# Kernel optimization log

Measured on AMD Instinct MI355X. Metric: run time of the kernel, lower is better.

## Reference

```python
import jax, jax.numpy as jnp
import numpy as np

B, S, D = 2, 1024, 4096
H, KV, HD = 32, 8, 128
GROUP = H // KV


def qlinear(x, w_int8, w_scale, bias):
    """Int8 dynamic-activation-quant linear: per-row activation scale, per-out-channel weight scale."""
    K = x.shape[-1]
    xf = x.reshape(-1, K)
    sx = jnp.max(jnp.abs(xf), axis=1, keepdims=True) / 127.0  # [M,1]
    sx = jnp.where(sx == 0, jnp.float32(1.0), sx)
    xi = jax.lax.stop_gradient(jnp.clip(jnp.round(xf / sx), -127.0, 127.0)).astype(jnp.int8)
    y = jnp.matmul(xi.astype(jnp.int32), w_int8.T.astype(jnp.int32)).astype(jnp.float32)  # int32 accum
    y = y * sx * w_scale[None, :]
    if bias is not None:
        y = y + bias
    return y.reshape(x.shape[:-1] + (w_int8.shape[0],))


def rope(t, c, s):
    half = t.shape[-1] // 2
    rot = jnp.concatenate([-t[..., half:], t[..., :half]], axis=-1)
    return t * c + rot * s


def setup_inputs() -> dict:
    key = jax.random.key(0)
    ks = jax.random.split(key, 10)
    x = jax.random.normal(ks[0], (B, S, D), dtype=jnp.float32)
    # RoPE tables (full-head_dim rotate-half convention)
    inv = 1.0 / (10000.0 ** (jnp.arange(0, HD, 2, dtype=jnp.float32) / HD))
    ang = jnp.arange(S, dtype=jnp.float32)[:, None] * inv[None, :]  # [S, HD/2]
    cos = jnp.concatenate([jnp.cos(ang), jnp.cos(ang)], axis=-1)
    sin = jnp.concatenate([jnp.sin(ang), jnp.sin(ang)], axis=-1)
    d_kv = KV * HD
    wq = jax.random.randint(ks[1], (H * HD, D), -127, 128, dtype=jnp.int32).astype(jnp.int8)
    wk = jax.random.randint(ks[2], (d_kv, D), -127, 128, dtype=jnp.int32).astype(jnp.int8)
    wv = jax.random.randint(ks[3], (d_kv, D), -127, 128, dtype=jnp.int32).astype(jnp.int8)
    wo = jax.random.randint(ks[4], (D, H * HD), -127, 128, dtype=jnp.int32).astype(jnp.int8)
    sc_in = jnp.float32(1.0 / (127.0 * np.sqrt(D)))
    sc_o = jnp.float32(1.0 / (127.0 * np.sqrt(H * HD)))
    sq = jnp.full((H * HD,), sc_in, dtype=jnp.float32)
    sk = jnp.full((d_kv,), sc_in, dtype=jnp.float32)
    sv = jnp.full((d_kv,), sc_in, dtype=jnp.float32)
    so = jnp.full((D,), sc_o, dtype=jnp.float32)
    bq = 0.01 * jax.random.normal(ks[5], (H * HD,), dtype=jnp.float32)
    bk = 0.01 * jax.random.normal(ks[6], (d_kv,), dtype=jnp.float32)
    bv = 0.01 * jax.random.normal(ks[7], (d_kv,), dtype=jnp.float32)
    return {"x": x, "cos": cos, "sin": sin, "wq": wq, "sq": sq, "bq": bq,
            "wk": wk, "sk": sk, "bk": bk, "wv": wv, "sv": sv, "bv": bv,
            "wo": wo, "so": so}


def reference(x, cos, sin, wq, sq, bq, wk, sk, bk, wv, sv, bv, wo, so):
    b, seq, _ = x.shape
    q = qlinear(x, wq, sq, bq).reshape(b, seq, H, HD)
    k = qlinear(x, wk, sk, bk).reshape(b, seq, KV, HD)
    v = qlinear(x, wv, sv, bv).reshape(b, seq, KV, HD)
    c = cos[:seq][None, :, None, :]
    s = sin[:seq][None, :, None, :]
    q = rope(q, c, s)
    k = rope(k, c, s)
    # start_pos=0 prefill: cache write then slice-back is identity -> use k, v directly.
    # GQA broadcast: q_head_to_kv_head = h // group_size
    idx = jnp.arange(H) // GROUP
    kf = k[:, :, idx, :]  # [b, seq, H, HD]
    vf = v[:, :, idx, :]
    scores = jnp.einsum('bqhd,bkhd->bhqk', q, kf) / jnp.sqrt(jnp.float32(HD))
    causal = jnp.tril(jnp.ones((seq, seq), dtype=bool))
    scores = jnp.where(causal[None, None, :, :], scores, jnp.float32(-jnp.inf))
    probs = jax.nn.softmax(scores, axis=-1)
    out = jnp.einsum('bhqk,bkhd->bqhd', probs, vf).reshape(b, seq, H * HD)
    return qlinear(out, wo, so, None)
```

## Files before the change

kernel.cpp:

```cpp
#include <hip/hip_runtime.h>


#define B_   2
#define S_   1024
#define D_   4096
#define H_   32
#define KV_  8
#define HD_  128
#define NR   (B_ * S_)
#define NQKV (H_*HD_ + 2*KV_*HD_)

#define KSTR 132
#define VSTR 68

typedef __attribute__((ext_vector_type(8))) short  short8;
typedef __attribute__((ext_vector_type(4))) float  f32x4;
typedef __attribute__((ext_vector_type(4))) int    int4v;

static __device__ __forceinline__ unsigned short f2bf(float f) {
    unsigned u = __builtin_bit_cast(unsigned, f);
    u += 0x7fffu + ((u >> 16) & 1u);
    return (unsigned short)(u >> 16);
}

static __device__ __forceinline__ void async_cp16(const void* g, void* l) {
    __builtin_amdgcn_global_load_lds(
        (const __attribute__((address_space(1))) void*)g,
        (__attribute__((address_space(3))) void*)l, 16, 0, 0);
}

__global__ __launch_bounds__(256) void quantize_rows_k(
    const float* __restrict__ X, signed char* __restrict__ Xq,
    float* __restrict__ sx_out)
{
    int row = blockIdx.x;
    const f32x4* xr = (const f32x4*)(X + (size_t)row * 4096);
    int t = threadIdx.x;

    f32x4 v[4];
    #pragma unroll
    for (int i = 0; i < 4; i++) v[i] = xr[t + i * 256];

    float m = 0.f;
    #pragma unroll
    for (int i = 0; i < 4; i++)
        #pragma unroll
        for (int j = 0; j < 4; j++) m = fmaxf(m, fabsf(v[i][j]));
    #pragma unroll
    for (int off = 32; off > 0; off >>= 1) m = fmaxf(m, __shfl_down(m, off, 64));
    __shared__ float red[4];
    if ((t & 63) == 0) red[t >> 6] = m;
    __syncthreads();
    float mm = fmaxf(fmaxf(red[0], red[1]), fmaxf(red[2], red[3]));
    float sx = mm / 127.0f;
    if (sx == 0.f) sx = 1.f;
    if (t == 0) sx_out[row] = sx;

    int* dst = (int*)(Xq + (size_t)row * 4096);
    #pragma unroll
    for (int i = 0; i < 4; i++) {
        int o = 0;
        #pragma unroll
        for (int j = 0; j < 4; j++) {
            float q = rintf(v[i][j] / sx);
            q = fminf(fmaxf(q, -127.f), 127.f);
            o |= (((int)q) & 0xff) << (j * 8);
        }
        dst[t + i * 256] = o;
    }
}

__global__ __launch_bounds__(256) void convert_all_w(
    const int* __restrict__ wq, const int* __restrict__ wk,
    const int* __restrict__ wv, const int* __restrict__ wo,
    signed char* __restrict__ Wqkv, signed char* __restrict__ Wo)
{
    int i = blockIdx.x * 256 + threadIdx.x;
    const int* src;
    signed char* dst;
    if (i < 1048576)      { src = wq + (size_t)i * 16;              dst = Wqkv + (size_t)i * 16; }
    else if (i < 1310720) { int j = i - 1048576; src = wk + (size_t)j * 16; dst = Wqkv + 16777216 + (size_t)j * 16; }
    else if (i < 1572864) { int j = i - 1310720; src = wv + (size_t)j * 16; dst = Wqkv + 20971520 + (size_t)j * 16; }
    else                  { int j = i - 1572864; src = wo + (size_t)j * 16; dst = Wo + (size_t)j * 16; }
    const int4v* s4 = (const int4v*)src;
    int4v a = s4[0], b = s4[1], c = s4[2], d = s4[3];
    int4v o;
    o[0] = (a[0]&0xff) | ((a[1]&0xff)<<8) | ((a[2]&0xff)<<16) | ((a[3]&0xff)<<24);
    o[1] = (b[0]&0xff) | ((b[1]&0xff)<<8) | ((b[2]&0xff)<<16) | ((b[3]&0xff)<<24);
    o[2] = (c[0]&0xff) | ((c[1]&0xff)<<8) | ((c[2]&0xff)<<16) | ((c[3]&0xff)<<24);
    o[3] = (d[0]&0xff) | ((d[1]&0xff)<<8) | ((d[2]&0xff)<<16) | ((d[3]&0xff)<<24);
    *(int4v*)dst = o;
}

template<int MODE>
__global__ __launch_bounds__(256) void gemm_i8_k(
    const signed char* __restrict__ A, const signed char* __restrict__ Bm,
    float* __restrict__ C, const float* __restrict__ rs,
    const float* __restrict__ cs, int K, int lda, int ldb, int ldc)
{
    __shared__ __align__(16) signed char As[128 * 128];
    __shared__ __align__(16) signed char Bs[128 * 128];

    int t    = threadIdx.x;
    int m0   = blockIdx.y * 128;
    int n0   = blockIdx.x * 128;
    int lane = t & 63;
    int w    = t >> 6;
    int wm   = (w >> 1) * 64;
    int wn   = (w & 1) * 64;
    int l15  = lane & 15;
    int quad = lane >> 4;

    int4v acc[4][4];
    #pragma unroll
    for (int i = 0; i < 4; i++)
        #pragma unroll
        for (int j = 0; j < 4; j++) { int4v z = {0,0,0,0}; acc[i][j] = z; }

    int cw   = w * 64 + lane;
    int smr  = cw >> 3;
    int scol = cw & 7;

    for (int k0 = 0; k0 < K; k0 += 128) {
        #pragma unroll
        for (int p = 0; p < 4; ++p) {
            int m  = p * 32 + smr;
            int kc = scol ^ (m & 7);
            const signed char* ga = A  + (size_t)(m0 + m) * lda + k0 + kc * 16;
            const signed char* gb = Bm + (size_t)(n0 + m) * ldb + k0 + kc * 16;
            async_cp16(ga, As + (p * 256 + w * 64) * 16);
            async_cp16(gb, Bs + (p * 256 + w * 64) * 16);
        }
        __syncthreads();

        #pragma unroll
        for (int ks = 0; ks < 2; ks++) {
            int4v af[4], bf[4];
            #pragma unroll
            for (int i = 0; i < 4; i++) {
                int ra = wm + i*16 + l15;
                int rb = wn + i*16 + l15;
                af[i] = *(const int4v*)&As[(ra * 8 + (((ks*4 + quad) ^ (ra & 7)))) * 16];
                bf[i] = *(const int4v*)&Bs[(rb * 8 + (((ks*4 + quad) ^ (rb & 7)))) * 16];
            }
            #pragma unroll
            for (int i = 0; i < 4; i++)
                #pragma unroll
                for (int j = 0; j < 4; j++)
                    acc[i][j] = __builtin_amdgcn_mfma_i32_16x16x64_i8(af[i], bf[j], acc[i][j], 0, 0, 0);
        }
        __syncthreads();
    }

    #pragma unroll
    for (int i = 0; i < 4; i++) {
        #pragma unroll
        for (int j = 0; j < 4; j++) {
            #pragma unroll
            for (int r = 0; r < 4; r++) {
                int row = m0 + wm + i*16 + quad*4 + r;
                int col = n0 + wn + j*16 + l15;
                float v = (float)acc[i][j][r];
                if (MODE == 3) v *= rs[row] * cs[col];
                C[(size_t)row * ldc + col] = v;
            }
        }
    }
}

__global__ __launch_bounds__(256) void derope_k(
    const float* __restrict__ Y, const float* __restrict__ sx,
    const float* __restrict__ sq, const float* __restrict__ bq,
    const float* __restrict__ sk, const float* __restrict__ bk,
    const float* __restrict__ sv, const float* __restrict__ bv,
    const float* __restrict__ cosb, const float* __restrict__ sinb,
    unsigned short* __restrict__ Q, unsigned short* __restrict__ Kb,
    unsigned short* __restrict__ Vt)
{
    const float qs = 0.08838834764831845f;
    int r = blockIdx.x;
    int b = r >> 10;
    int s = r & (S_ - 1);
    float sxr = sx[r];
    const float* yr = Y + (size_t)r * NQKV;
    int t = threadIdx.x;

    for (int p = t; p < H_ * 64; p += 256) {
        int h = p >> 6, d = p & 63;
        int ca = h * HD_ + d;
        float a  = yr[ca]      * sxr * sq[ca]      + bq[ca];
        float b2 = yr[ca + 64] * sxr * sq[ca + 64] + bq[ca + 64];
        float c  = cosb[s * HD_ + d], sn = sinb[s * HD_ + d];
        size_t base = (((size_t)(b * H_ + h)) * S_ + s) * HD_;
        Q[base + d]      = f2bf((a * c - b2 * sn) * qs);
        Q[base + d + 64] = f2bf((b2 * c + a * sn) * qs);
    }
    for (int p = t; p < KV_ * 64; p += 256) {
        int kv = p >> 6, d = p & 63;
        int ci = kv * HD_ + d;
        int ca = H_ * HD_ + ci;
        float a  = yr[ca]      * sxr * sk[ci]      + bk[ci];
        float b2 = yr[ca + 64] * sxr * sk[ci + 64] + bk[ci + 64];
        float c  = cosb[s * HD_ + d], sn = sinb[s * HD_ + d];
        size_t base = (((size_t)(b * KV_ + kv)) * S_ + s) * HD_;
        Kb[base + d]      = f2bf(a * c - b2 * sn);
        Kb[base + d + 64] = f2bf(b2 * c + a * sn);
    }
    for (int p = t; p < KV_ * HD_; p += 256) {
        int kv = p >> 7, d = p & 127;
        int ci = kv * HD_ + d;
        int ca = H_ * HD_ + KV_ * HD_ + ci;
        float v = yr[ca] * sxr * sv[ci] + bv[ci];
        size_t idx = (((size_t)(b * KV_ + kv)) * HD_ + d) * S_ + s;
        Vt[idx] = f2bf(v);
    }
}

__global__ __launch_bounds__(256) void flash_attn_k(
    const unsigned short* __restrict__ Qg,
    const unsigned short* __restrict__ Kg,
    const unsigned short* __restrict__ Vg,
    float* __restrict__ O)
{
    __shared__ __align__(16) unsigned short Ks[64 * KSTR];
    __shared__ __align__(16) unsigned short Vs[HD_ * VSTR];

    int pair = blockIdx.x;
    int qt   = 15 - blockIdx.y;
    int b    = pair >> 5;
    int kv   = (pair & 31) >> 2;

    const unsigned short* Qb = Qg + ((size_t)pair * S_ + qt * 64) * HD_;
    const unsigned short* Kbp = Kg + ((size_t)(b * KV_ + kv)) * (S_ * HD_);
    const unsigned short* Vb = Vg + ((size_t)(b * KV_ + kv)) * (HD_ * S_);

    int t    = threadIdx.x;
    int lane = t & 63;
    int w    = t >> 6;
    int l15  = lane & 15;
    int quad = lane >> 4;

    short8 qf[4];
    #pragma unroll
    for (int ks = 0; ks < 4; ks++)
        qf[ks] = *(const short8*)(Qb + (size_t)(w*16 + l15) * HD_ + ks*32 + quad*8);

    f32x4 oacc[8];
    #pragma unroll
    for (int n = 0; n < 8; n++) { f32x4 z = {0.f,0.f,0.f,0.f}; oacc[n] = z; }
    float mrow[4], lrow[4];
    #pragma unroll
    for (int r = 0; r < 4; r++) { mrow[r] = -1e30f; lrow[r] = 0.f; }

    int kr4 = t >> 4, kc = t & 15;
    int vr4 = t >> 3, vc = t & 7;

    for (int j = 0; j <= qt; ++j) {
        int k0 = j * 64;
        __syncthreads();

        #pragma unroll
        for (int p = 0; p < 4; ++p) {
            int krow = p * 16 + kr4;
            short8 kd = *(const short8*)(Kbp + (size_t)(k0 + krow) * HD_ + kc * 8);
            *(short8*)&Ks[krow * KSTR + kc * 8] = kd;
            int vrow = p * 32 + vr4;
            short8 vd = *(const short8*)(Vb + (size_t)vrow * S_ + k0 + vc * 8);
            *(short8*)&Vs[vrow * VSTR + vc * 8] = vd;
        }
        __syncthreads();

        f32x4 sacc[4];
        #pragma unroll
        for (int n = 0; n < 4; n++) { f32x4 z = {0.f,0.f,0.f,0.f}; sacc[n] = z; }
        #pragma unroll
        for (int n = 0; n < 4; n++) {
            #pragma unroll
            for (int ks = 0; ks < 4; ks++) {
                short8 kf = *(const short8*)&Ks[(n*16 + l15) * KSTR + ks*32 + quad*8];
                sacc[n] = __builtin_amdgcn_mfma_f32_16x16x32_bf16(qf[ks], kf, sacc[n], 0, 0, 0);
            }
        }

        if (j == qt) {
            #pragma unroll
            for (int n = 0; n < 4; n++)
                #pragma unroll
                for (int r = 0; r < 4; r++) {
                    int qrow = w*16 + quad*4 + r;
                    int kcol = n*16 + l15;
                    if (kcol > qrow) sacc[n][r] = -1e30f;
                }
        }

        #pragma unroll
        for (int r = 0; r < 4; r++) {
            float mx = fmaxf(fmaxf(sacc[0][r], sacc[1][r]), fmaxf(sacc[2][r], sacc[3][r]));
            mx = fmaxf(mx, __shfl_xor(mx, 1, 64));
            mx = fmaxf(mx, __shfl_xor(mx, 2, 64));
            mx = fmaxf(mx, __shfl_xor(mx, 4, 64));
            mx = fmaxf(mx, __shfl_xor(mx, 8, 64));
            float mnew = fmaxf(mrow[r], mx);
            float alpha = __expf(mrow[r] - mnew);
            mrow[r] = mnew;
            float s = 0.f;
            #pragma unroll
            for (int n = 0; n < 4; n++) {
                float e = __expf(sacc[n][r] - mnew);
                sacc[n][r] = e;
                s += e;
            }
            s += __shfl_xor(s, 1, 64);
            s += __shfl_xor(s, 2, 64);
            s += __shfl_xor(s, 4, 64);
            s += __shfl_xor(s, 8, 64);
            lrow[r] = lrow[r] * alpha + s;
            #pragma unroll
            for (int n = 0; n < 8; n++) oacc[n][r] *= alpha;
        }

        __syncthreads();

        unsigned short* Ps = Ks;
        #pragma unroll
        for (int n = 0; n < 4; n++)
            #pragma unroll
            for (int r = 0; r < 4; r++)
                Ps[(w*16 + quad*4 + r) * KSTR + n*16 + l15] = f2bf(sacc[n][r]);

        short8 pf[2];
        #pragma unroll
        for (int ks = 0; ks < 2; ks++)
            pf[ks] = *(const short8*)&Ps[(w*16 + l15) * KSTR + ks*32 + quad*8];
        #pragma unroll
        for (int n = 0; n < 8; n++) {
            #pragma unroll
            for (int ks = 0; ks < 2; ks++) {
                short8 vf = *(const short8*)&Vs[(n*16 + l15) * VSTR + ks*32 + quad*8];
                oacc[n] = __builtin_amdgcn_mfma_f32_16x16x32_bf16(pf[ks], vf, oacc[n], 0, 0, 0);
            }
        }
    }

    float* Ob = O + ((size_t)(b * S_ + qt * 64)) * (H_*HD_) + (pair & 31) * HD_;
    #pragma unroll
    for (int r = 0; r < 4; r++) {
        float inv = 1.0f / lrow[r];
        int row = w*16 + quad*4 + r;
        #pragma unroll
        for (int n = 0; n < 8; n++)
            Ob[(size_t)row * (H_*HD_) + n*16 + l15] = oacc[n][r] * inv;
    }
}

extern "C" void kernel_launch(void* const* d_in, const int* in_sizes, int n_in,
                              void* d_out, int out_size, void* d_ws, size_t ws_size,
                              hipStream_t stream)
{
    (void)in_sizes; (void)n_in; (void)out_size; (void)ws_size;
    const float* x    = (const float*)d_in[0];
    const float* cosb = (const float*)d_in[1];
    const float* sinb = (const float*)d_in[2];
    const int*   wq   = (const int*)d_in[3];
    const float* sq   = (const float*)d_in[4];
    const float* bq   = (const float*)d_in[5];
    const int*   wk   = (const int*)d_in[6];
    const float* sk   = (const float*)d_in[7];
    const float* bk   = (const float*)d_in[8];
    const int*   wv   = (const int*)d_in[9];
    const float* sv   = (const float*)d_in[10];
    const float* bv   = (const float*)d_in[11];
    const int*   wo   = (const int*)d_in[12];
    const float* so   = (const float*)d_in[13];
    float* out = (float*)d_out;
    char*  ws  = (char*)d_ws;

    signed char*    Xi   = (signed char*)(ws + 0);
    float*          Y    = (float*)(ws + 8388608ull);
    signed char*    Wqkv = (signed char*)(ws + 58720256ull);
    signed char*    Oi   = (signed char*)(ws + 58720256ull);
    signed char*    Wo   = (signed char*)(ws + 83886080ull);
    unsigned short* Q    = (unsigned short*)(ws + 100663296ull);
    unsigned short* Kb   = (unsigned short*)(ws + 117440512ull);
    unsigned short* Vt   = (unsigned short*)(ws + 121634816ull);
    float*          O    = (float*)(ws + 125829120ull);
    float*          sx   = (float*)(ws + 159383552ull);
    float*          sxo  = (float*)(ws + 159391744ull);

    quantize_rows_k<<<dim3(NR), dim3(256), 0, stream>>>(x, Xi, sx);

    convert_all_w<<<dim3(10240), dim3(256), 0, stream>>>(wq, wk, wv, wo, Wqkv, Wo);

    gemm_i8_k<0><<<dim3(48,16,1), dim3(256), 0, stream>>>(
        Xi, Wqkv, Y, nullptr, nullptr, D_, D_, D_, NQKV);

    derope_k<<<dim3(NR), dim3(256), 0, stream>>>(
        Y, sx, sq, bq, sk, bk, sv, bv, cosb, sinb, Q, Kb, Vt);

    flash_attn_k<<<dim3(64, 16), dim3(256), 0, stream>>>(Q, Kb, Vt, O);

    quantize_rows_k<<<dim3(NR), dim3(256), 0, stream>>>(O, Oi, sxo);

    gemm_i8_k<3><<<dim3(32,16,1), dim3(256), 0, stream>>>(
        Oi, Wo, out, sxo, so, D_, D_, D_, D_);
}
```

Before: 428.5 us.

## Restructure flash attention with 128-key tiles, register prefetch, swizzled LDS and paired q-tiles

Each attention block now handles two query tiles (tp and 15-tp) so causal work is balanced across blocks, and the grid is halved. Key tiles grow from 64 to 128 rows. The next K/V tile is prefetched into registers while the current tile is computed, and an XOR swizzle replaces the padded LDS strides to avoid bank conflicts. This raises register and LDS use (64KB shared) and processes some fully masked columns on the diagonal 128-wide tile. That trades occupancy and extra masked work for less global-load latency and fewer launches of unbalanced blocks.

```diff
diff --git a/kernel.cpp b/kernel.cpp
--- a/kernel.cpp
+++ b/kernel.cpp
@@ -10,12 +10,11 @@
 #define NR   (B_ * S_)
 #define NQKV (H_*HD_ + 2*KV_*HD_)
 
-#define KSTR 132
-#define VSTR 68
-
 typedef __attribute__((ext_vector_type(8))) short  short8;
 typedef __attribute__((ext_vector_type(4))) float  f32x4;
 typedef __attribute__((ext_vector_type(4))) int    int4v;
+
+#define FA_SW(c, r) (((c) & 8) | (((c) & 7) ^ ((r) & 7)))
 
 static __device__ __forceinline__ unsigned short f2bf(float f) {
     unsigned u = __builtin_bit_cast(unsigned, f);
@@ -216,140 +215,169 @@
     }
 }
 
-__global__ __launch_bounds__(256) void flash_attn_k(
+__global__ __launch_bounds__(256, 2) void flash_attn_k(
     const unsigned short* __restrict__ Qg,
     const unsigned short* __restrict__ Kg,
     const unsigned short* __restrict__ Vg,
     float* __restrict__ O)
 {
-    __shared__ __align__(16) unsigned short Ks[64 * KSTR];
-    __shared__ __align__(16) unsigned short Vs[HD_ * VSTR];
+    __shared__ __align__(16) unsigned short Ks[128 * 128];
+    __shared__ __align__(16) unsigned short Vs[128 * 128];
 
     int pair = blockIdx.x;
-    int qt   = 15 - blockIdx.y;
+    int tp   = blockIdx.y;
     int b    = pair >> 5;
     int kv   = (pair & 31) >> 2;
 
-    const unsigned short* Qb = Qg + ((size_t)pair * S_ + qt * 64) * HD_;
     const unsigned short* Kbp = Kg + ((size_t)(b * KV_ + kv)) * (S_ * HD_);
-    const unsigned short* Vb = Vg + ((size_t)(b * KV_ + kv)) * (HD_ * S_);
+    const unsigned short* Vb  = Vg + ((size_t)(b * KV_ + kv)) * (HD_ * S_);
 
     int t    = threadIdx.x;
     int lane = t & 63;
     int w    = t >> 6;
     int l15  = lane & 15;
     int quad = lane >> 4;
-
-    short8 qf[4];
-    #pragma unroll
-    for (int ks = 0; ks < 4; ks++)
-        qf[ks] = *(const short8*)(Qb + (size_t)(w*16 + l15) * HD_ + ks*32 + quad*8);
-
-    f32x4 oacc[8];
-    #pragma unroll
-    for (int n = 0; n < 8; n++) { f32x4 z = {0.f,0.f,0.f,0.f}; oacc[n] = z; }
-    float mrow[4], lrow[4];
-    #pragma unroll
-    for (int r = 0; r < 4; r++) { mrow[r] = -1e30f; lrow[r] = 0.f; }
-
-    int kr4 = t >> 4, kc = t & 15;
-    int vr4 = t >> 3, vc = t & 7;
-
-    for (int j = 0; j <= qt; ++j) {
-        int k0 = j * 64;
-        __syncthreads();
-
-        #pragma unroll
-        for (int p = 0; p < 4; ++p) {
-            int krow = p * 16 + kr4;
-            short8 kd = *(const short8*)(Kbp + (size_t)(k0 + krow) * HD_ + kc * 8);
-            *(short8*)&Ks[krow * KSTR + kc * 8] = kd;
-            int vrow = p * 32 + vr4;
-            short8 vd = *(const short8*)(Vb + (size_t)vrow * S_ + k0 + vc * 8);
-            *(short8*)&Vs[vrow * VSTR + vc * 8] = vd;
-        }
-        __syncthreads();
-
-        f32x4 sacc[4];
-        #pragma unroll
-        for (int n = 0; n < 4; n++) { f32x4 z = {0.f,0.f,0.f,0.f}; sacc[n] = z; }
-        #pragma unroll
-        for (int n = 0; n < 4; n++) {
-            #pragma unroll
-            for (int ks = 0; ks < 4; ks++) {
-                short8 kf = *(const short8*)&Ks[(n*16 + l15) * KSTR + ks*32 + quad*8];
-                sacc[n] = __builtin_amdgcn_mfma_f32_16x16x32_bf16(qf[ks], kf, sacc[n], 0, 0, 0);
-            }
-        }
-
-        if (j == qt) {
-            #pragma unroll
-            for (int n = 0; n < 4; n++)
+    int trow = t >> 4;
+    int tcol = t & 15;
+
+    short8 kreg[8], vreg[8];
+    #pragma unroll
+    for (int p = 0; p < 8; ++p) {
+        int row = p * 16 + trow;
+        kreg[p] = *(const short8*)(Kbp + (size_t)row * HD_ + tcol * 8);
+        vreg[p] = *(const short8*)(Vb  + (size_t)row * S_  + tcol * 8);
+    }
+
+    #pragma unroll
+    for (int phase = 0; phase < 2; ++phase) {
+        int qt   = phase ? (15 - tp) : tp;
+        int n128 = (qt + 2) >> 1;
+        const unsigned short* Qb = Qg + ((size_t)pair * S_ + qt * 64) * HD_;
+
+        short8 qf[4];
+        #pragma unroll
+        for (int ks = 0; ks < 4; ks++)
+            qf[ks] = *(const short8*)(Qb + (size_t)(w*16 + l15) * HD_ + ks*32 + quad*8);
+
+        f32x4 oacc[8];
+        #pragma unroll
+        for (int n = 0; n < 8; n++) { f32x4 z = {0.f,0.f,0.f,0.f}; oacc[n] = z; }
+        float mrow[4], lrow[4];
+        #pragma unroll
+        for (int r = 0; r < 4; r++) { mrow[r] = -1e30f; lrow[r] = 0.f; }
+
+        for (int j = 0; j < n128; ++j) {
+            __syncthreads();
+
+            #pragma unroll
+            for (int p = 0; p < 8; ++p) {
+                int row = p * 16 + trow;
+                int c = FA_SW(tcol, row);
+                *(short8*)&Ks[row * 128 + c * 8] = kreg[p];
+                *(short8*)&Vs[row * 128 + c * 8] = vreg[p];
+            }
+            __syncthreads();
+
+            int k0n = (j + 1 < n128) ? (j + 1) * 128 : (phase == 0 ? 0 : -1);
+            if (k0n >= 0) {
+                #pragma unroll
+                for (int p = 0; p < 8; ++p) {
+                    int row = p * 16 + trow;
+                    kreg[p] = *(const short8*)(Kbp + (size_t)(k0n + row) * HD_ + tcol * 8);
+                    vreg[p] = *(const short8*)(Vb  + (size_t)row * S_ + k0n + tcol * 8);
+                }
+            }
+
+            f32x4 sacc[8];
+            #pragma unroll
+            for (int n = 0; n < 8; n++) { f32x4 z = {0.f,0.f,0.f,0.f}; sacc[n] = z; }
+            #pragma unroll
+            for (int n = 0; n < 8; n++) {
+                int row = n*16 + l15;
+                #pragma unroll
+                for (int ks = 0; ks < 4; ks++) {
+                    short8 kf = *(const short8*)&Ks[row * 128 + FA_SW(ks*4 + quad, row) * 8];
+                    sacc[n] = __builtin_amdgcn_mfma_f32_16x16x32_bf16(qf[ks], kf, sacc[n], 0, 0, 0);
+                }
+            }
+
+            if (j == n128 - 1) {
+                int k0 = j * 128;
+                #pragma unroll
+                for (int n = 0; n < 8; n++)
+                    #pragma unroll
+                    for (int r = 0; r < 4; r++) {
+                        int kcol = k0 + n*16 + l15;
+                        int qrow = qt*64 + w*16 + quad*4 + r;
+                        if (kcol > qrow) sacc[n][r] = -1e30f;
+                    }
+            }
+
+            #pragma unroll
+            for (int r = 0; r < 4; r++) {
+                float mx = sacc[0][r];
+                #pragma unroll
+                for (int n = 1; n < 8; n++) mx = fmaxf(mx, sacc[n][r]);
+                mx = fmaxf(mx, __shfl_xor(mx, 1, 64));
+                mx = fmaxf(mx, __shfl_xor(mx, 2, 64));
+                mx = fmaxf(mx, __shfl_xor(mx, 4, 64));
+                mx = fmaxf(mx, __shfl_xor(mx, 8, 64));
+                float mnew = fmaxf(mrow[r], mx);
+                float alpha = __expf(mrow[r] - mnew);
+                mrow[r] = mnew;
+                float s = 0.f;
+                #pragma unroll
+                for (int n = 0; n < 8; n++) {
+                    float e = __expf(sacc[n][r] - mnew);
+                    sacc[n][r] = e;
+                    s += e;
+                }
+                s += __shfl_xor(s, 1, 64);
+                s += __shfl_xor(s, 2, 64);
+                s += __shfl_xor(s, 4, 64);
+                s += __shfl_xor(s, 8, 64);
+                lrow[r] = lrow[r] * alpha + s;
+                #pragma unroll
+                for (int n = 0; n < 8; n++) oacc[n][r] *= alpha;
+            }
+
+            __syncthreads();
+
+            #pragma unroll
+            for (int n = 0; n < 8; n++)
                 #pragma unroll
                 for (int r = 0; r < 4; r++) {
                     int qrow = w*16 + quad*4 + r;
                     int kcol = n*16 + l15;
-                    if (kcol > qrow) sacc[n][r] = -1e30f;
+                    Ks[qrow * 128 + FA_SW(kcol >> 3, qrow) * 8 + (kcol & 7)] = f2bf(sacc[n][r]);
                 }
-        }
-
+
+            short8 pf[4];
+            #pragma unroll
+            for (int ks = 0; ks < 4; ks++) {
+                int row = w*16 + l15;
+                pf[ks] = *(const short8*)&Ks[row * 128 + FA_SW(ks*4 + quad, row) * 8];
+            }
+            #pragma unroll
+            for (int n = 0; n < 8; n++) {
+                int row = n*16 + l15;
+                #pragma unroll
+                for (int ks = 0; ks < 4; ks++) {
+                    short8 vf = *(const short8*)&Vs[row * 128 + FA_SW(ks*4 + quad, row) * 8];
+                    oacc[n] = __builtin_amdgcn_mfma_f32_16x16x32_bf16(pf[ks], vf, oacc[n], 0, 0, 0);
+                }
+            }
+        }
+
+        float* Ob = O + ((size_t)(b * S_ + qt * 64)) * (H_*HD_) + (pair & 31) * HD_;
         #pragma unroll
         for (int r = 0; r < 4; r++) {
-            float mx = fmaxf(fmaxf(sacc[0][r], sacc[1][r]), fmaxf(sacc[2][r], sacc[3][r]));
-            mx = fmaxf(mx, __shfl_xor(mx, 1, 64));
-            mx = fmaxf(mx, __shfl_xor(mx, 2, 64));
-            mx = fmaxf(mx, __shfl_xor(mx, 4, 64));
-            mx = fmaxf(mx, __shfl_xor(mx, 8, 64));
-            float mnew = fmaxf(mrow[r], mx);
-            float alpha = __expf(mrow[r] - mnew);
-            mrow[r] = mnew;
-            float s = 0.f;
-            #pragma unroll
-            for (int n = 0; n < 4; n++) {
-                float e = __expf(sacc[n][r] - mnew);
-                sacc[n][r] = e;
-                s += e;
-            }
-            s += __shfl_xor(s, 1, 64);
-            s += __shfl_xor(s, 2, 64);
-            s += __shfl_xor(s, 4, 64);
-            s += __shfl_xor(s, 8, 64);
-            lrow[r] = lrow[r] * alpha + s;
-            #pragma unroll
-            for (int n = 0; n < 8; n++) oacc[n][r] *= alpha;
-        }
-
-        __syncthreads();
-
-        unsigned short* Ps = Ks;
-        #pragma unroll
-        for (int n = 0; n < 4; n++)
-            #pragma unroll
-            for (int r = 0; r < 4; r++)
-                Ps[(w*16 + quad*4 + r) * KSTR + n*16 + l15] = f2bf(sacc[n][r]);
-
-        short8 pf[2];
-        #pragma unroll
-        for (int ks = 0; ks < 2; ks++)
-            pf[ks] = *(const short8*)&Ps[(w*16 + l15) * KSTR + ks*32 + quad*8];
-        #pragma unroll
-        for (int n = 0; n < 8; n++) {
-            #pragma unroll
-            for (int ks = 0; ks < 2; ks++) {
-                short8 vf = *(const short8*)&Vs[(n*16 + l15) * VSTR + ks*32 + quad*8];
-                oacc[n] = __builtin_amdgcn_mfma_f32_16x16x32_bf16(pf[ks], vf, oacc[n], 0, 0, 0);
-            }
-        }
-    }
-
-    float* Ob = O + ((size_t)(b * S_ + qt * 64)) * (H_*HD_) + (pair & 31) * HD_;
-    #pragma unroll
-    for (int r = 0; r < 4; r++) {
-        float inv = 1.0f / lrow[r];
-        int row = w*16 + quad*4 + r;
-        #pragma unroll
-        for (int n = 0; n < 8; n++)
-            Ob[(size_t)row * (H_*HD_) + n*16 + l15] = oacc[n][r] * inv;
+            float inv = 1.0f / lrow[r];
+            int row = w*16 + quad*4 + r;
+            #pragma unroll
+            for (int n = 0; n < 8; n++)
+                Ob[(size_t)row * (H_*HD_) + n*16 + l15] = oacc[n][r] * inv;
+        }
     }
 }
 
@@ -397,7 +425,7 @@
     derope_k<<<dim3(NR), dim3(256), 0, stream>>>(
         Y, sx, sq, bq, sk, bk, sv, bv, cosb, sinb, Q, Kb, Vt);
 
-    flash_attn_k<<<dim3(64, 16), dim3(256), 0, stream>>>(Q, Kb, Vt, O);
+    flash_attn_k<<<dim3(64, 8), dim3(256), 0, stream>>>(Q, Kb, Vt, O);
 
     quantize_rows_k<<<dim3(NR), dim3(256), 0, stream>>>(O, Oi, sxo);
 
```

Measured after the change: 412.6 us. 3.7% less time.
